# Performance work log

Hardware: AMD Instinct MI355X
Metric: run time of the kernel (lower is better)

Reference implementation:

```python
import jax, jax.numpy as jnp
import numpy as np

MARGIN = 1.0
EPS = 1e-05
B = 8192
D = 128
NUM_CLASSES = 256


def setup_inputs() -> dict:
    key = jax.random.key(0)
    k1, k2 = jax.random.split(key)
    feature = jax.random.normal(k1, (B, D), dtype=jnp.float32)
    label = jax.random.randint(k2, (B,), 0, NUM_CLASSES, dtype=jnp.int32)
    return {"feature": feature, "label": label}


def reference(feature, label):
    # Pairwise Euclidean distance matrix: ||x_i||^2 + ||x_j||^2 - 2 x_i.x_j + eps, then sqrt
    sq = jnp.sum(feature * feature, axis=1, keepdims=True)  # [B, 1]
    dist = jnp.sqrt(jnp.maximum(sq + sq.T - 2.0 * (feature @ feature.T) + EPS, 0.0))  # [B, B]

    same = label[:, None] == label[None, :]  # [B, B] bool, includes self on diagonal
    inf = jnp.array(jnp.inf, dtype=dist.dtype)

    # Original sorts each row and takes same[1]: the SECOND smallest same-label distance
    # (the smallest is the anchor itself, distance sqrt(eps)).
    d_same = jnp.where(same, dist, inf)
    two_smallest = -jax.lax.top_k(-d_same, 2)[0]  # [B, 2], ascending smallest two
    pos = two_smallest[:, 1]  # nearest positive excluding self

    # diff.min(): hardest (closest) negative per row
    neg = jnp.min(jnp.where(same, inf, dist), axis=1)

    hinge = jnp.maximum(MARGIN + pos - neg, 0.0)
    return jnp.mean(hinge)
```

## Files before the change

### kernel.cpp

```cpp
#include <hip/hip_runtime.h>
#include <math.h>


#define BN 8192
#define MARGIN_F 1.0f
#define EPS_F 1e-5f

typedef __attribute__((ext_vector_type(8))) short short8;
typedef __attribute__((ext_vector_type(4))) float floatx4;

__device__ __forceinline__ unsigned short bf16_rne(float x, float& r) {
    unsigned u = __float_as_uint(x);
    u += 0x7FFF + ((u >> 16) & 1);
    unsigned short h = (unsigned short)(u >> 16);
    r = __uint_as_float(((unsigned)h) << 16);
    return h;
}

__global__ __launch_bounds__(256) void prep_kernel(const float* __restrict__ f,
                                                   const int* __restrict__ lbl,
                                                   short8* __restrict__ fbT,
                                                   float2* __restrict__ lsq,
                                                   float* __restrict__ g_acc,
                                                   unsigned* __restrict__ counter) {
    int gid = blockIdx.x * 256 + threadIdx.x;
    if (gid == 0) { *g_acc = 0.f; *counter = 0u; }
    int row = gid >> 3, part = gid & 7;
    const float4* f4 = (const float4*)f + (size_t)row * 32 + part * 4;
    float s = 0.f;
#pragma unroll
    for (int cc = 0; cc < 2; ++cc) {
        float4 v0 = f4[cc * 2], v1 = f4[cc * 2 + 1];
        float r0, r1, r2, r3, r4, r5, r6, r7;
        short8 o;
        o[0] = (short)bf16_rne(v0.x, r0);
        o[1] = (short)bf16_rne(v0.y, r1);
        o[2] = (short)bf16_rne(v0.z, r2);
        o[3] = (short)bf16_rne(v0.w, r3);
        o[4] = (short)bf16_rne(v1.x, r4);
        o[5] = (short)bf16_rne(v1.y, r5);
        o[6] = (short)bf16_rne(v1.z, r6);
        o[7] = (short)bf16_rne(v1.w, r7);
        fbT[(size_t)(part * 2 + cc) * BN + row] = o;
        s += r0 * r0 + r1 * r1 + r2 * r2 + r3 * r3 +
             r4 * r4 + r5 * r5 + r6 * r6 + r7 * r7;
    }
    s += __shfl_xor(s, 1, 8);
    s += __shfl_xor(s, 2, 8);
    s += __shfl_xor(s, 4, 8);
    if (part == 0) {
        float2 p;
        p.x = s;
        p.y = __int_as_float(lbl[row]);
        lsq[row] = p;
    }
}

__device__ __forceinline__ void stage_tile(const short8* __restrict__ fbT,
                                           short8* tile, int j0, int wv, int lane) {
#pragma unroll
    for (int it = 0; it < 2; ++it) {
        int s = wv * 128 + it * 64;
        int kc = (s >> 5) + (lane >> 5);
        int col = lane & 31;
        const short8* g = fbT + ((size_t)kc * BN + j0 + col);
        __builtin_amdgcn_global_load_lds(
            (const __attribute__((address_space(1))) void*)g,
            (__attribute__((address_space(3))) void*)(tile + s),
            16, 0, 0);
    }
}

__global__ __launch_bounds__(256, 2) void work_kernel(const short8* __restrict__ fbT,
                                                      const float2* __restrict__ lsq,
                                                      float* __restrict__ part_n1,
                                                      float* __restrict__ part_s1,
                                                      float* __restrict__ part_s2) {
    const int t = threadIdx.x;
    const int lane = t & 63;
    const int wv = t >> 6;
    const int q = lane >> 4, c = lane & 15;
    const int bid = blockIdx.x;

    __shared__ short8 Bt[2][512];
    __shared__ float2 lsq_sh[512];

    const int i0 = (bid & 31) * 256 + wv * 64;
    const int g = bid >> 5;
    const int jb = g * 512;

    stage_tile(fbT, Bt[0], jb, wv, lane);

    lsq_sh[t] = lsq[jb + t];
    lsq_sh[t + 256] = lsq[jb + t + 256];

    short8 a[4][4];
#pragma unroll
    for (int mf = 0; mf < 4; ++mf) {
        int row = i0 + mf * 16 + c;
#pragma unroll
        for (int ks = 0; ks < 4; ++ks)
            a[mf][ks] = fbT[(size_t)(ks * 4 + q) * BN + row];
    }
    int li[4][4];
#pragma unroll
    for (int mf = 0; mf < 4; ++mf)
#pragma unroll
        for (int rg = 0; rg < 4; ++rg)
            li[mf][rg] = __float_as_int(lsq[i0 + mf * 16 + q * 4 + rg].y);

    float n1[4][4], s1[4][4], s2[4][4];
#pragma unroll
    for (int mf = 0; mf < 4; ++mf)
#pragma unroll
        for (int rg = 0; rg < 4; ++rg) {
            n1[mf][rg] = INFINITY;
            s1[mf][rg] = INFINITY;
            s2[mf][rg] = INFINITY;
        }

    __syncthreads();

    for (int jt = 0; jt < 16; ++jt) {
        const short8* cur = Bt[jt & 1];
        const int j0 = jb + jt * 32;
        if (jt < 15) stage_tile(fbT, Bt[1 - (jt & 1)], j0 + 32, wv, lane);

        int ljv[2]; float sjv[2];
#pragma unroll
        for (int nf = 0; nf < 2; ++nf) {
            float2 p = lsq_sh[jt * 32 + nf * 16 + c];
            sjv[nf] = p.x;
            ljv[nf] = __float_as_int(p.y);
        }

        floatx4 acc[4][2];
#pragma unroll
        for (int mf = 0; mf < 4; ++mf)
#pragma unroll
            for (int nf = 0; nf < 2; ++nf) acc[mf][nf] = (floatx4)0.f;

#pragma unroll
        for (int ks = 0; ks < 4; ++ks) {
            short8 b[2];
#pragma unroll
            for (int nf = 0; nf < 2; ++nf)
                b[nf] = cur[(ks * 4 + q) * 32 + nf * 16 + c];
#pragma unroll
            for (int mf = 0; mf < 4; ++mf)
#pragma unroll
                for (int nf = 0; nf < 2; ++nf)
                    acc[mf][nf] = __builtin_amdgcn_mfma_f32_16x16x32_bf16(
                        a[mf][ks], b[nf], acc[mf][nf], 0, 0, 0);
        }

#pragma unroll
        for (int nf = 0; nf < 2; ++nf) {
#pragma unroll
            for (int mf = 0; mf < 4; ++mf)
#pragma unroll
                for (int rg = 0; rg < 4; ++rg) {
                    float v = fmaf(-2.0f, acc[mf][nf][rg], sjv[nf]);
                    bool same = (li[mf][rg] == ljv[nf]);
                    float vd = same ? INFINITY : v;
                    float vs = same ? v : INFINITY;
                    n1[mf][rg] = fminf(n1[mf][rg], vd);
                    s2[mf][rg] = fminf(s2[mf][rg], fmaxf(s1[mf][rg], vs));
                    s1[mf][rg] = fminf(s1[mf][rg], vs);
                }
        }
        __syncthreads();
    }

#pragma unroll
    for (int m = 1; m < 16; m <<= 1) {
#pragma unroll
        for (int mf = 0; mf < 4; ++mf)
#pragma unroll
            for (int rg = 0; rg < 4; ++rg) {
                n1[mf][rg] = fminf(n1[mf][rg], __shfl_xor(n1[mf][rg], m, 16));
                float o1 = __shfl_xor(s1[mf][rg], m, 16);
                float o2 = __shfl_xor(s2[mf][rg], m, 16);
                float hi = fminf(fmaxf(s1[mf][rg], o1), fminf(s2[mf][rg], o2));
                s1[mf][rg] = fminf(s1[mf][rg], o1);
                s2[mf][rg] = hi;
            }
    }
    if (c == 0) {
#pragma unroll
        for (int mf = 0; mf < 4; ++mf)
#pragma unroll
            for (int rg = 0; rg < 4; ++rg) {
                int idx = g * BN + i0 + mf * 16 + q * 4 + rg;
                part_n1[idx] = n1[mf][rg];
                part_s1[idx] = s1[mf][rg];
                part_s2[idx] = s2[mf][rg];
            }
    }
}

__global__ __launch_bounds__(128) void merge_kernel(const float* __restrict__ part_n1,
                                                    const float* __restrict__ part_s1,
                                                    const float* __restrict__ part_s2,
                                                    const float2* __restrict__ lsq,
                                                    float* __restrict__ g_acc,
                                                    unsigned* __restrict__ counter,
                                                    float* __restrict__ out) {
    int r = blockIdx.x * 128 + threadIdx.x;
    float n = INFINITY, s1 = INFINITY, s2 = INFINITY;
#pragma unroll
    for (int k = 0; k < 16; ++k) {
        n = fminf(n, part_n1[k * BN + r]);
        float a1 = part_s1[k * BN + r];
        float a2 = part_s2[k * BN + r];
        s2 = fminf(fmaxf(s1, a1), fminf(s2, a2));
        s1 = fminf(s1, a1);
    }
    float si = lsq[r].x;
    float pos = sqrtf(fmaxf(si + s2 + EPS_F, 0.f));
    float neg = sqrtf(fmaxf(si + n + EPS_F, 0.f));
    float h = fmaxf(MARGIN_F + pos - neg, 0.f);
    __shared__ float red[2];
#pragma unroll
    for (int m = 32; m >= 1; m >>= 1) h += __shfl_down(h, m, 64);
    if ((threadIdx.x & 63) == 0) red[threadIdx.x >> 6] = h;
    __syncthreads();
    if (threadIdx.x == 0) {
        atomicAdd(g_acc, red[0] + red[1]);
        __threadfence();
        unsigned old = atomicAdd(counter, 1u);
        if (old == 63u) {
            float tot = atomicAdd(g_acc, 0.0f);
            out[0] = tot / (float)BN;
        }
    }
}

extern "C" void kernel_launch(void* const* d_in, const int* in_sizes, int n_in,
                              void* d_out, int out_size, void* d_ws, size_t ws_size,
                              hipStream_t stream) {
    const float* f = (const float*)d_in[0];
    const int* lbl = (const int*)d_in[1];
    char* ws = (char*)d_ws;
    float2* lsq = (float2*)ws;
    short8* fbT = (short8*)(ws + 65536);
    float* part_n1 = (float*)(ws + 65536 + 2097152);
    float* part_s1 = (float*)(ws + 65536 + 2097152 + 524288);
    float* part_s2 = (float*)(ws + 65536 + 2097152 + 1048576);
    float* g_acc = (float*)(ws + 65536 + 2097152 + 1572864);
    unsigned* counter = (unsigned*)(g_acc + 1);
    float* out = (float*)d_out;

    prep_kernel<<<256, 256, 0, stream>>>(f, lbl, fbT, lsq, g_acc, counter);
    work_kernel<<<512, 256, 0, stream>>>(fbT, lsq, part_n1, part_s1, part_s2);
    merge_kernel<<<64, 128, 0, stream>>>(part_n1, part_s1, part_s2, lsq, g_acc, counter, out);
}
```

Before: 94.69 us.

## Replace top-two positive tracking with explicit self-exclusion and drop LDS staging

```diff
diff --git a/kernel.cpp b/kernel.cpp
--- a/kernel.cpp
+++ b/kernel.cpp
@@ -56,168 +56,153 @@
     }
 }
 
-__device__ __forceinline__ void stage_tile(const short8* __restrict__ fbT,
-                                           short8* tile, int j0, int wv, int lane) {
-#pragma unroll
-    for (int it = 0; it < 2; ++it) {
-        int s = wv * 128 + it * 64;
-        int kc = (s >> 5) + (lane >> 5);
-        int col = lane & 31;
-        const short8* g = fbT + ((size_t)kc * BN + j0 + col);
-        __builtin_amdgcn_global_load_lds(
-            (const __attribute__((address_space(1))) void*)g,
-            (__attribute__((address_space(3))) void*)(tile + s),
-            16, 0, 0);
-    }
-}
-
-__global__ __launch_bounds__(256, 2) void work_kernel(const short8* __restrict__ fbT,
+template <bool DIAG>
+__device__ __forceinline__ void jt_loop(const short8* __restrict__ bp,
+                                        const float2* lsq_sh,
+                                        const short8 a[2][4], const int li[2][4],
+                                        float n1[2][4], float ss1[2][4],
+                                        int c, int q, int i0, int jb) {
+    for (int jt = 0; jt < 16; ++jt) {
+        short8 b[4][2];
+#pragma unroll
+        for (int ks = 0; ks < 4; ++ks)
+#pragma unroll
+            for (int nf = 0; nf < 2; ++nf)
+                b[ks][nf] = bp[(size_t)ks * 4 * BN + jt * 32 + nf * 16];
+
+        int ljv[2]; float sjv[2];
+#pragma unroll
+        for (int nf = 0; nf < 2; ++nf) {
+            float2 p = lsq_sh[jt * 32 + nf * 16 + c];
+            sjv[nf] = p.x;
+            ljv[nf] = __float_as_int(p.y);
+        }
+
+        int dd = DIAG ? ((i0 + q * 4) - (jb + jt * 32 + c)) : 0;
+
+        floatx4 acc[2][2];
+#pragma unroll
+        for (int mf = 0; mf < 2; ++mf)
+#pragma unroll
+            for (int nf = 0; nf < 2; ++nf) acc[mf][nf] = (floatx4)0.f;
+
+#pragma unroll
+        for (int ks = 0; ks < 4; ++ks)
+#pragma unroll
+            for (int mf = 0; mf < 2; ++mf)
+#pragma unroll
+                for (int nf = 0; nf < 2; ++nf)
+                    acc[mf][nf] = __builtin_amdgcn_mfma_f32_16x16x32_bf16(
+                        a[mf][ks], b[ks][nf], acc[mf][nf], 0, 0, 0);
+
+#pragma unroll
+        for (int nf = 0; nf < 2; ++nf)
+#pragma unroll
+            for (int mf = 0; mf < 2; ++mf)
+#pragma unroll
+                for (int rg = 0; rg < 4; ++rg) {
+                    float v = fmaf(-2.0f, acc[mf][nf][rg], sjv[nf]);
+                    bool same = (li[mf][rg] == ljv[nf]);
+                    float vd = same ? INFINITY : v;
+                    n1[mf][rg] = fminf(n1[mf][rg], vd);
+                    bool excl = same;
+                    if (DIAG) excl = same && (dd != (nf * 16 - mf * 16 - rg));
+                    float vs = excl ? v : INFINITY;
+                    ss1[mf][rg] = fminf(ss1[mf][rg], vs);
+                }
+    }
+}
+
+__global__ __launch_bounds__(256, 4) void work_kernel(const short8* __restrict__ fbT,
                                                       const float2* __restrict__ lsq,
                                                       float* __restrict__ part_n1,
-                                                      float* __restrict__ part_s1,
-                                                      float* __restrict__ part_s2) {
+                                                      float* __restrict__ part_p1) {
     const int t = threadIdx.x;
     const int lane = t & 63;
     const int wv = t >> 6;
     const int q = lane >> 4, c = lane & 15;
     const int bid = blockIdx.x;
 
-    __shared__ short8 Bt[2][512];
     __shared__ float2 lsq_sh[512];
 
-    const int i0 = (bid & 31) * 256 + wv * 64;
-    const int g = bid >> 5;
+    const int ib = bid & 63;
+    const int g = bid >> 6;
+    const int i0 = ib * 128 + wv * 32;
     const int jb = g * 512;
-
-    stage_tile(fbT, Bt[0], jb, wv, lane);
+    const bool diag = ((ib >> 2) == g);
 
     lsq_sh[t] = lsq[jb + t];
     lsq_sh[t + 256] = lsq[jb + t + 256];
 
-    short8 a[4][4];
-#pragma unroll
-    for (int mf = 0; mf < 4; ++mf) {
+    short8 a[2][4];
+#pragma unroll
+    for (int mf = 0; mf < 2; ++mf) {
         int row = i0 + mf * 16 + c;
 #pragma unroll
         for (int ks = 0; ks < 4; ++ks)
             a[mf][ks] = fbT[(size_t)(ks * 4 + q) * BN + row];
     }
-    int li[4][4];
-#pragma unroll
-    for (int mf = 0; mf < 4; ++mf)
+    int li[2][4];
+#pragma unroll
+    for (int mf = 0; mf < 2; ++mf)
 #pragma unroll
         for (int rg = 0; rg < 4; ++rg)
             li[mf][rg] = __float_as_int(lsq[i0 + mf * 16 + q * 4 + rg].y);
 
-    float n1[4][4], s1[4][4], s2[4][4];
-#pragma unroll
-    for (int mf = 0; mf < 4; ++mf)
+    float n1[2][4], ss1[2][4];
+#pragma unroll
+    for (int mf = 0; mf < 2; ++mf)
 #pragma unroll
         for (int rg = 0; rg < 4; ++rg) {
             n1[mf][rg] = INFINITY;
-            s1[mf][rg] = INFINITY;
-            s2[mf][rg] = INFINITY;
+            ss1[mf][rg] = INFINITY;
         }
 
     __syncthreads();
 
-    for (int jt = 0; jt < 16; ++jt) {
-        const short8* cur = Bt[jt & 1];
-        const int j0 = jb + jt * 32;
-        if (jt < 15) stage_tile(fbT, Bt[1 - (jt & 1)], j0 + 32, wv, lane);
-
-        int ljv[2]; float sjv[2];
-#pragma unroll
-        for (int nf = 0; nf < 2; ++nf) {
-            float2 p = lsq_sh[jt * 32 + nf * 16 + c];
-            sjv[nf] = p.x;
-            ljv[nf] = __float_as_int(p.y);
-        }
-
-        floatx4 acc[4][2];
-#pragma unroll
-        for (int mf = 0; mf < 4; ++mf)
-#pragma unroll
-            for (int nf = 0; nf < 2; ++nf) acc[mf][nf] = (floatx4)0.f;
-
-#pragma unroll
-        for (int ks = 0; ks < 4; ++ks) {
-            short8 b[2];
-#pragma unroll
-            for (int nf = 0; nf < 2; ++nf)
-                b[nf] = cur[(ks * 4 + q) * 32 + nf * 16 + c];
-#pragma unroll
-            for (int mf = 0; mf < 4; ++mf)
-#pragma unroll
-                for (int nf = 0; nf < 2; ++nf)
-                    acc[mf][nf] = __builtin_amdgcn_mfma_f32_16x16x32_bf16(
-                        a[mf][ks], b[nf], acc[mf][nf], 0, 0, 0);
-        }
-
-#pragma unroll
-        for (int nf = 0; nf < 2; ++nf) {
-#pragma unroll
-            for (int mf = 0; mf < 4; ++mf)
-#pragma unroll
-                for (int rg = 0; rg < 4; ++rg) {
-                    float v = fmaf(-2.0f, acc[mf][nf][rg], sjv[nf]);
-                    bool same = (li[mf][rg] == ljv[nf]);
-                    float vd = same ? INFINITY : v;
-                    float vs = same ? v : INFINITY;
-                    n1[mf][rg] = fminf(n1[mf][rg], vd);
-                    s2[mf][rg] = fminf(s2[mf][rg], fmaxf(s1[mf][rg], vs));
-                    s1[mf][rg] = fminf(s1[mf][rg], vs);
-                }
-        }
-        __syncthreads();
-    }
+    const short8* bp = fbT + (size_t)q * BN + jb + c;
+    if (diag)
+        jt_loop<true>(bp, lsq_sh, a, li, n1, ss1, c, q, i0, jb);
+    else
+        jt_loop<false>(bp, lsq_sh, a, li, n1, ss1, c, q, i0, jb);
 
 #pragma unroll
     for (int m = 1; m < 16; m <<= 1) {
 #pragma unroll
-        for (int mf = 0; mf < 4; ++mf)
+        for (int mf = 0; mf < 2; ++mf)
 #pragma unroll
             for (int rg = 0; rg < 4; ++rg) {
                 n1[mf][rg] = fminf(n1[mf][rg], __shfl_xor(n1[mf][rg], m, 16));
-                float o1 = __shfl_xor(s1[mf][rg], m, 16);
-                float o2 = __shfl_xor(s2[mf][rg], m, 16);
-                float hi = fminf(fmaxf(s1[mf][rg], o1), fminf(s2[mf][rg], o2));
-                s1[mf][rg] = fminf(s1[mf][rg], o1);
-                s2[mf][rg] = hi;
+                ss1[mf][rg] = fminf(ss1[mf][rg], __shfl_xor(ss1[mf][rg], m, 16));
             }
     }
     if (c == 0) {
 #pragma unroll
-        for (int mf = 0; mf < 4; ++mf)
+        for (int mf = 0; mf < 2; ++mf)
 #pragma unroll
             for (int rg = 0; rg < 4; ++rg) {
                 int idx = g * BN + i0 + mf * 16 + q * 4 + rg;
                 part_n1[idx] = n1[mf][rg];
-                part_s1[idx] = s1[mf][rg];
-                part_s2[idx] = s2[mf][rg];
+                part_p1[idx] = ss1[mf][rg];
             }
     }
 }
 
 __global__ __launch_bounds__(128) void merge_kernel(const float* __restrict__ part_n1,
-                                                    const float* __restrict__ part_s1,
-                                                    const float* __restrict__ part_s2,
+                                                    const float* __restrict__ part_p1,
                                                     const float2* __restrict__ lsq,
                                                     float* __restrict__ g_acc,
                                                     unsigned* __restrict__ counter,
                                                     float* __restrict__ out) {
     int r = blockIdx.x * 128 + threadIdx.x;
-    float n = INFINITY, s1 = INFINITY, s2 = INFINITY;
+    float n = INFINITY, ss = INFINITY;
 #pragma unroll
     for (int k = 0; k < 16; ++k) {
         n = fminf(n, part_n1[k * BN + r]);
-        float a1 = part_s1[k * BN + r];
-        float a2 = part_s2[k * BN + r];
-        s2 = fminf(fmaxf(s1, a1), fminf(s2, a2));
-        s1 = fminf(s1, a1);
+        ss = fminf(ss, part_p1[k * BN + r]);
     }
     float si = lsq[r].x;
-    float pos = sqrtf(fmaxf(si + s2 + EPS_F, 0.f));
+    float pos = sqrtf(fmaxf(si + ss + EPS_F, 0.f));
     float neg = sqrtf(fmaxf(si + n + EPS_F, 0.f));
     float h = fmaxf(MARGIN_F + pos - neg, 0.f);
     __shared__ float red[2];
@@ -245,13 +230,12 @@
     float2* lsq = (float2*)ws;
     short8* fbT = (short8*)(ws + 65536);
     float* part_n1 = (float*)(ws + 65536 + 2097152);
-    float* part_s1 = (float*)(ws + 65536 + 2097152 + 524288);
-    float* part_s2 = (float*)(ws + 65536 + 2097152 + 1048576);
-    float* g_acc = (float*)(ws + 65536 + 2097152 + 1572864);
+    float* part_p1 = (float*)(ws + 65536 + 2097152 + 524288);
+    float* g_acc = (float*)(ws + 65536 + 2097152 + 1048576);
     unsigned* counter = (unsigned*)(g_acc + 1);
     float* out = (float*)d_out;
 
     prep_kernel<<<256, 256, 0, stream>>>(f, lbl, fbT, lsq, g_acc, counter);
-    work_kernel<<<512, 256, 0, stream>>>(fbT, lsq, part_n1, part_s1, part_s2);
-    merge_kernel<<<64, 128, 0, stream>>>(part_n1, part_s1, part_s2, lsq, g_acc, counter, out);
-}
+    work_kernel<<<1024, 256, 0, stream>>>(fbT, lsq, part_n1, part_p1);
+    merge_kernel<<<64, 128, 0, stream>>>(part_n1, part_p1, lsq, g_acc, counter, out);
+}
```

After: 85.97 us. -9.2%, faster.
